# Kernel tuning notes

Measured on AMD Instinct MI355X. Metric: run time of the kernel, lower is better.

The kernel has to match this reference:

```python
import jax, jax.numpy as jnp
import numpy as np

NUM_EMBEDDINGS = 512
EMBEDDING_DIM = 64
COMMITMENT_COST = 0.25


def setup_inputs() -> dict:
    key = jax.random.key(0)
    k1, k2 = jax.random.split(key)
    inputs = jax.random.normal(k1, (64, 32, 32, EMBEDDING_DIM), dtype=jnp.float32)
    # nn.Embedding weight init: uniform(-1/K, 1/K)
    codebook = jax.random.uniform(
        k2, (NUM_EMBEDDINGS, EMBEDDING_DIM), dtype=jnp.float32,
        minval=-1.0 / NUM_EMBEDDINGS, maxval=1.0 / NUM_EMBEDDINGS)
    return {"inputs": inputs, "codebook": codebook}


def reference(inputs, codebook):
    D = codebook.shape[1]
    K = codebook.shape[0]
    flat = inputs.reshape(-1, D)  # [N, D]
    # Squared euclidean distances (argmin-equivalent to torch.cdist output)
    d2 = (jnp.sum(flat * flat, axis=1, keepdims=True)
          - 2.0 * (flat @ codebook.T)
          + jnp.sum(codebook * codebook, axis=1))  # [N, K]
    idx = jnp.argmin(d2, axis=1)  # [N]
    # Gather codebook rows (== one-hot @ codebook in the original)
    quantized = codebook[idx].reshape(inputs.shape)
    e_latent_loss = jnp.mean((jax.lax.stop_gradient(quantized) - inputs) ** 2)
    q_latent_loss = jnp.mean((quantized - jax.lax.stop_gradient(inputs)) ** 2)
    loss = q_latent_loss + COMMITMENT_COST * e_latent_loss
    # Straight-through estimator
    quantized_st = inputs + jax.lax.stop_gradient(quantized - inputs)
    # Perplexity from code usage histogram (== mean of one-hot encodings)
    n = flat.shape[0]
    avg_probs = jnp.zeros((K,), dtype=jnp.float32).at[idx].add(1.0) / n
    perplexity = jnp.exp(-jnp.sum(avg_probs * jnp.log(avg_probs + 1e-10)))
    encoding_indices = idx[:, None]  # [N, 1] to match torch unsqueeze(1)
    return (loss, quantized_st, perplexity, encoding_indices)
```

## Files before the change

kernel.cpp:

```cpp
#include <hip/hip_runtime.h>
#include <math.h>

#define K_EMB 512
#define DIM 64
#define NVEC 65536
#define OUT_LOSS 0
#define OUT_Q 1
#define OUT_PERP (1 + NVEC * DIM)
#define OUT_IDX (1 + NVEC * DIM + 1)
#define EPS2 1e-4f
#define FIX_CAP 16

typedef __attribute__((ext_vector_type(8))) short short8;
typedef __attribute__((ext_vector_type(4))) float float4v;


__device__ __forceinline__ unsigned short bf16_rn(float f) {
    unsigned u = __float_as_uint(f);
    return (unsigned short)((u + 0x7FFFu + ((u >> 16) & 1u)) >> 16);
}

__device__ __forceinline__ float np_pairwise8_sq(const float* v) {
    float r[8];
#pragma unroll
    for (int j = 0; j < 8; ++j) r[j] = __fmul_rn(v[j], v[j]);
#pragma unroll
    for (int i = 8; i < 64; i += 8) {
#pragma unroll
        for (int j = 0; j < 8; ++j) r[j] = __fadd_rn(r[j], __fmul_rn(v[i + j], v[i + j]));
    }
    return __fadd_rn(__fadd_rn(__fadd_rn(r[0], r[1]), __fadd_rn(r[2], r[3])),
                     __fadd_rn(__fadd_rn(r[4], r[5]), __fadd_rn(r[6], r[7])));
}

__global__ void vq_frag(const float* __restrict__ codebook, float* __restrict__ csq,
                        unsigned short* __restrict__ ahi, unsigned short* __restrict__ alo,
                        float4* __restrict__ csqf, unsigned* __restrict__ hist,
                        double* __restrict__ sse64) {
    const int id = blockIdx.x * 256 + threadIdx.x;
    const int t = id >> 7, step = (id >> 6) & 1, lane = id & 63;
    const int m = t * 16 + (lane & 15);
    const int kb = step * 32 + (lane >> 4) * 8;
    const float* src = codebook + (m << 6) + kb;
    short8 h, l;
#pragma unroll
    for (int j = 0; j < 8; ++j) {
        float f = src[j];
        unsigned short hv = bf16_rn(f);
        float lof = f - __uint_as_float(((unsigned)hv) << 16);
        h[j] = (short)hv;
        l[j] = (short)bf16_rn(lof);
    }
    const int fo = ((t * 2 + step) * 64 + lane) * 8;
    *(short8*)(ahi + fo) = h;
    *(short8*)(alo + fo) = l;
    if (step == 0) {
        const int k0 = t * 16 + (lane >> 4) * 4;
        csqf[t * 64 + lane] = make_float4(np_pairwise8_sq(codebook + (size_t)(k0 + 0) * 64),
                                          np_pairwise8_sq(codebook + (size_t)(k0 + 1) * 64),
                                          np_pairwise8_sq(codebook + (size_t)(k0 + 2) * 64),
                                          np_pairwise8_sq(codebook + (size_t)(k0 + 3) * 64));
    }
    if (id < 512) {
        csq[id] = np_pairwise8_sq(codebook + ((size_t)id << 6));
        hist[id] = 0u;
    }
    if (id >= 512 && id < 576) sse64[id - 512] = 0.0;
}

__launch_bounds__(256, 4)
__global__ void vq_main(const float* __restrict__ inputs, const float* __restrict__ codebook,
                        const float* __restrict__ csq, const unsigned short* __restrict__ ahi,
                        const unsigned short* __restrict__ alo, const float4* __restrict__ csqf,
                        unsigned* __restrict__ hist, double* __restrict__ sse64,
                        float* __restrict__ out) {
    __shared__ __align__(16) float s_x[64 * 68];
    __shared__ float s_A[64];
    __shared__ unsigned long long s_t1[4][64];
    __shared__ unsigned long long s_t2[4][64];
    __shared__ unsigned long long s_e[64];
    __shared__ int s_fix[FIX_CAP];
    __shared__ int s_nfix;
    __shared__ float s_w[4];

    const int tid = threadIdx.x;
    const int wave = tid >> 6, lane = tid & 63;
    const int vbase = blockIdx.x * 64;

    if (tid == 0) s_nfix = 0;

    {
        const float4* src = (const float4*)(inputs + ((size_t)vbase << 6));
#pragma unroll
        for (int i = 0; i < 4; ++i) {
            const int f = i * 256 + tid;
            float4 v = src[f];
            *(float4*)&s_x[(f >> 4) * 68 + (f & 15) * 4] = v;
        }
    }
    __syncthreads();

    if (tid < 64) s_A[tid] = np_pairwise8_sq(&s_x[tid * 68]);
    __syncthreads();

    short8 bhi[4][2], blo[4][2];
#pragma unroll
    for (int vt = 0; vt < 4; ++vt) {
        const int vrow = vt * 16 + (lane & 15);
#pragma unroll
        for (int step = 0; step < 2; ++step) {
            const int kb = step * 32 + (lane >> 4) * 8;
            float4 f0 = *(const float4*)&s_x[vrow * 68 + kb];
            float4 f1 = *(const float4*)&s_x[vrow * 68 + kb + 4];
            const float fs[8] = {f0.x, f0.y, f0.z, f0.w, f1.x, f1.y, f1.z, f1.w};
            short8 h, l;
#pragma unroll
            for (int j = 0; j < 8; ++j) {
                unsigned short hv = bf16_rn(fs[j]);
                float lof = fs[j] - __uint_as_float(((unsigned)hv) << 16);
                h[j] = (short)hv;
                l[j] = (short)bf16_rn(lof);
            }
            bhi[vt][step] = h;
            blo[vt][step] = l;
        }
    }

    unsigned long long e1[4] = {~0ULL, ~0ULL, ~0ULL, ~0ULL};
    unsigned long long e2[4] = {~0ULL, ~0ULL, ~0ULL, ~0ULL};

#pragma unroll 2
    for (int tt = 0; tt < 8; ++tt) {
        const int t = wave * 8 + tt;
        const int fo0 = ((t * 2 + 0) * 64 + lane) * 8;
        const int fo1 = ((t * 2 + 1) * 64 + lane) * 8;
        short8 ah0 = *(const short8*)(ahi + fo0);
        short8 ah1 = *(const short8*)(ahi + fo1);
        short8 al0 = *(const short8*)(alo + fo0);
        short8 al1 = *(const short8*)(alo + fo1);
        float4 cs = csqf[t * 64 + lane];
        const float csr[4] = {cs.x, cs.y, cs.z, cs.w};
#pragma unroll
        for (int vt = 0; vt < 4; ++vt) {
            float4v acc = {0.f, 0.f, 0.f, 0.f};
            acc = __builtin_amdgcn_mfma_f32_16x16x32_bf16(ah0, bhi[vt][0], acc, 0, 0, 0);
            acc = __builtin_amdgcn_mfma_f32_16x16x32_bf16(ah1, bhi[vt][1], acc, 0, 0, 0);
            acc = __builtin_amdgcn_mfma_f32_16x16x32_bf16(ah0, blo[vt][0], acc, 0, 0, 0);
            acc = __builtin_amdgcn_mfma_f32_16x16x32_bf16(ah1, blo[vt][1], acc, 0, 0, 0);
            acc = __builtin_amdgcn_mfma_f32_16x16x32_bf16(al0, bhi[vt][0], acc, 0, 0, 0);
            acc = __builtin_amdgcn_mfma_f32_16x16x32_bf16(al1, bhi[vt][1], acc, 0, 0, 0);
            const float Avt = s_A[vt * 16 + (lane & 15)];
#pragma unroll
            for (int r = 0; r < 4; ++r) {
                float d2 = __fadd_rn(__fsub_rn(Avt, __fmul_rn(2.0f, acc[r])), csr[r]);
                const unsigned k = (unsigned)(t * 16 + (lane >> 4) * 4 + r);
                unsigned long long e = ((unsigned long long)__float_as_uint(d2) << 32) | k;
                if (e < e1[vt]) { e2[vt] = e1[vt]; e1[vt] = e; }
                else if (e < e2[vt]) e2[vt] = e;
            }
        }
    }

#pragma unroll
    for (int vt = 0; vt < 4; ++vt) {
#pragma unroll
        for (int off = 16; off <= 32; off <<= 1) {
            unsigned long long o1 = __shfl_xor(e1[vt], off);
            unsigned long long o2 = __shfl_xor(e2[vt], off);
            if (o1 < e1[vt]) { e2[vt] = (e1[vt] < o2) ? e1[vt] : o2; e1[vt] = o1; }
            else if (o1 < e2[vt]) e2[vt] = o1;
        }
        if (lane < 16) {
            s_t1[wave][vt * 16 + lane] = e1[vt];
            s_t2[wave][vt * 16 + lane] = e2[vt];
        }
    }
    __syncthreads();

    if (tid < 64) {
        unsigned long long E1 = ~0ULL, E2 = ~0ULL;
#pragma unroll
        for (int w = 0; w < 4; ++w) {
            unsigned long long a = s_t1[w][tid], b = s_t2[w][tid];
            if (a < E1) { E2 = (E1 < b) ? E1 : b; E1 = a; }
            else if (a < E2) E2 = a;
        }
        s_e[tid] = E1;
        float b1 = __uint_as_float((unsigned)(E1 >> 32));
        float b2 = __uint_as_float((unsigned)(E2 >> 32));
        if (__fsub_rn(b2, b1) <= EPS2) {
            int pos = atomicAdd(&s_nfix, 1);
            if (pos < FIX_CAP) s_fix[pos] = tid;
        }
    }
    __syncthreads();

    {
        int nf = s_nfix; if (nf > FIX_CAP) nf = FIX_CAP;
        for (int f = wave; f < nf; f += 4) {
            const int vloc = s_fix[f];
            const float* xr = &s_x[vloc * 68];
            const float A = s_A[vloc];
            unsigned long long best = ~0ULL;
#pragma unroll 1
            for (int r8 = 0; r8 < 8; ++r8) {
                const int k = lane * 8 + r8;
                const float* c = codebook + (k << 6);
                float p[8] = {0.f, 0.f, 0.f, 0.f, 0.f, 0.f, 0.f, 0.f};
#pragma unroll
                for (int ii = 0; ii < 64; ii += 8)
#pragma unroll
                    for (int j = 0; j < 8; ++j)
                        p[j] = __builtin_fmaf(xr[ii + j], c[ii + j], p[j]);
                float dot = __fadd_rn(__fadd_rn(__fadd_rn(p[0], p[1]), __fadd_rn(p[2], p[3])),
                                      __fadd_rn(__fadd_rn(p[4], p[5]), __fadd_rn(p[6], p[7])));
                float d2 = __fadd_rn(__fsub_rn(A, __fmul_rn(2.0f, dot)), csq[k]);
                unsigned long long e = ((unsigned long long)__float_as_uint(d2) << 32) | (unsigned)k;
                if (e < best) best = e;
            }
#pragma unroll
            for (int off = 32; off > 0; off >>= 1) {
                unsigned long long o = __shfl_down(best, off);
                if (o < best) best = o;
            }
            if (lane == 0) s_e[vloc] = best;
        }
    }
    __syncthreads();

    if (tid < 64) {
        const unsigned kf = (unsigned)s_e[tid];
        out[OUT_IDX + vbase + tid] = (float)kf;
        atomicAdd(&hist[kf], 1u);
    }
    {
        float4* dst = (float4*)(out + OUT_Q + ((size_t)vbase << 6));
        float es = 0.f;
#pragma unroll
        for (int i = 0; i < 4; ++i) {
            const int f = i * 256 + tid;
            const int row = f >> 4, col = (f & 15) * 4;
            const unsigned k = (unsigned)s_e[row];
            float4 qv = *(const float4*)(codebook + ((size_t)k << 6) + col);
            dst[f] = qv;
            float4 xv = *(const float4*)&s_x[row * 68 + col];
            float d0 = qv.x - xv.x; es = __builtin_fmaf(d0, d0, es);
            float d1 = qv.y - xv.y; es = __builtin_fmaf(d1, d1, es);
            float d2 = qv.z - xv.z; es = __builtin_fmaf(d2, d2, es);
            float d3 = qv.w - xv.w; es = __builtin_fmaf(d3, d3, es);
        }
#pragma unroll
        for (int off = 32; off > 0; off >>= 1) es += __shfl_down(es, off);
        if (lane == 0) s_w[wave] = es;
    }
    __syncthreads();
    if (tid == 0)
        atomicAdd(&sse64[blockIdx.x & 63],
                  (double)(((s_w[0] + s_w[1]) + (s_w[2] + s_w[3]))));
}

__global__ void vq_final(const unsigned* __restrict__ hist, const double* __restrict__ sse64,
                         float* __restrict__ out) {
    __shared__ float s_wsm[8];
    const int k = threadIdx.x;
    float pr = (float)hist[k] / 65536.0f;
    float v = __fmul_rn(pr, logf(__fadd_rn(pr, 1e-10f)));
#pragma unroll
    for (int off = 32; off > 0; off >>= 1) v += __shfl_down(v, off);
    if ((k & 63) == 0) s_wsm[k >> 6] = v;
    __syncthreads();
    if (k == 0) {
        float S = 0.f;
#pragma unroll
        for (int i = 0; i < 8; ++i) S += s_wsm[i];
        out[OUT_PERP] = expf(-S);
        double sv = 0.0;
        for (int i = 0; i < 64; ++i) sv += sse64[i];
        float m = (float)(sv / 4194304.0);
        out[OUT_LOSS] = __fadd_rn(m, __fmul_rn(0.25f, m));
    }
}

extern "C" void kernel_launch(void* const* d_in, const int* in_sizes, int n_in,
                              void* d_out, int out_size, void* d_ws, size_t ws_size,
                              hipStream_t stream) {
    const float* inputs   = (const float*)d_in[0];
    const float* codebook = (const float*)d_in[1];
    float* out = (float*)d_out;
    float*          csq   = (float*)d_ws;
    double*         sse64 = (double*)((char*)d_ws + 2048);
    unsigned*       hist  = (unsigned*)((char*)d_ws + 2560);
    unsigned short* ahi   = (unsigned short*)((char*)d_ws + 4608);
    unsigned short* alo   = (unsigned short*)((char*)d_ws + 70144);
    float4*         csqf  = (float4*)((char*)d_ws + 135680);

    vq_frag<<<16, 256, 0, stream>>>(codebook, csq, ahi, alo, csqf, hist, sse64);
    vq_main<<<1024, 256, 0, stream>>>(inputs, codebook, csq, ahi, alo, csqf, hist, sse64, out);
    vq_final<<<1, 512, 0, stream>>>(hist, sse64, out);
}
```

Before: 155.1 us.

## Halve vectors per block in main kernel and split codebook prep into dedicated block

The main kernel now processes 32 vectors per block instead of 64 and launches twice as many blocks, so more blocks spread across the CUs. Each wave still streams all codebook fragments, so global/L2 traffic for codebook fragments doubles relative to the MFMA work. The prep kernel moves the codebook norm computation into a separate extra block that computes each norm once and builds the packed norm array from shared memory, instead of recomputing norms redundantly, and vectorises the fragment loads. The fixup path (not fully shown) presumably still works with the smaller tile.

```diff
diff --git a/kernel.cpp b/kernel.cpp
--- a/kernel.cpp
+++ b/kernel.cpp
@@ -37,35 +37,46 @@
                         unsigned short* __restrict__ ahi, unsigned short* __restrict__ alo,
                         float4* __restrict__ csqf, unsigned* __restrict__ hist,
                         double* __restrict__ sse64) {
-    const int id = blockIdx.x * 256 + threadIdx.x;
-    const int t = id >> 7, step = (id >> 6) & 1, lane = id & 63;
-    const int m = t * 16 + (lane & 15);
-    const int kb = step * 32 + (lane >> 4) * 8;
-    const float* src = codebook + (m << 6) + kb;
-    short8 h, l;
-#pragma unroll
-    for (int j = 0; j < 8; ++j) {
-        float f = src[j];
-        unsigned short hv = bf16_rn(f);
-        float lof = f - __uint_as_float(((unsigned)hv) << 16);
-        h[j] = (short)hv;
-        l[j] = (short)bf16_rn(lof);
-    }
-    const int fo = ((t * 2 + step) * 64 + lane) * 8;
-    *(short8*)(ahi + fo) = h;
-    *(short8*)(alo + fo) = l;
-    if (step == 0) {
-        const int k0 = t * 16 + (lane >> 4) * 4;
-        csqf[t * 64 + lane] = make_float4(np_pairwise8_sq(codebook + (size_t)(k0 + 0) * 64),
-                                          np_pairwise8_sq(codebook + (size_t)(k0 + 1) * 64),
-                                          np_pairwise8_sq(codebook + (size_t)(k0 + 2) * 64),
-                                          np_pairwise8_sq(codebook + (size_t)(k0 + 3) * 64));
-    }
-    if (id < 512) {
-        csq[id] = np_pairwise8_sq(codebook + ((size_t)id << 6));
-        hist[id] = 0u;
-    }
-    if (id >= 512 && id < 576) sse64[id - 512] = 0.0;
+    const int tid = threadIdx.x;
+    if (blockIdx.x < 16) {
+        const int id = blockIdx.x * 256 + tid;
+        const int t = id >> 7, step = (id >> 6) & 1, lane = id & 63;
+        const int m = t * 16 + (lane & 15);
+        const int kb = step * 32 + (lane >> 4) * 8;
+        const float4* src = (const float4*)(codebook + (m << 6) + kb);
+        float4 f0 = src[0], f1 = src[1];
+        const float fs[8] = {f0.x, f0.y, f0.z, f0.w, f1.x, f1.y, f1.z, f1.w};
+        short8 h, l;
+#pragma unroll
+        for (int j = 0; j < 8; ++j) {
+            unsigned short hv = bf16_rn(fs[j]);
+            float lof = fs[j] - __uint_as_float(((unsigned)hv) << 16);
+            h[j] = (short)hv;
+            l[j] = (short)bf16_rn(lof);
+        }
+        const int fo = ((t * 2 + step) * 64 + lane) * 8;
+        *(short8*)(ahi + fo) = h;
+        *(short8*)(alo + fo) = l;
+    } else {
+        __shared__ float s_csq[512];
+#pragma unroll
+        for (int r = 0; r < 2; ++r) {
+            const int k = tid + 256 * r;
+            float v = np_pairwise8_sq(codebook + ((size_t)k << 6));
+            s_csq[k] = v;
+            csq[k] = v;
+            hist[k] = 0u;
+        }
+        if (tid < 64) sse64[tid] = 0.0;
+        __syncthreads();
+#pragma unroll
+        for (int i = 0; i < 8; ++i) {
+            const int id = i * 256 + tid;
+            const int t = id >> 6, lane = id & 63;
+            const int k0 = t * 16 + (lane >> 4) * 4;
+            csqf[id] = make_float4(s_csq[k0], s_csq[k0 + 1], s_csq[k0 + 2], s_csq[k0 + 3]);
+        }
+    }
 }
 
 __launch_bounds__(256, 4)
@@ -74,25 +85,25 @@
                         const unsigned short* __restrict__ alo, const float4* __restrict__ csqf,
                         unsigned* __restrict__ hist, double* __restrict__ sse64,
                         float* __restrict__ out) {
-    __shared__ __align__(16) float s_x[64 * 68];
-    __shared__ float s_A[64];
-    __shared__ unsigned long long s_t1[4][64];
-    __shared__ unsigned long long s_t2[4][64];
-    __shared__ unsigned long long s_e[64];
+    __shared__ __align__(16) float s_x[32 * 68];
+    __shared__ float s_A[32];
+    __shared__ unsigned long long s_t1[4][32];
+    __shared__ unsigned long long s_t2[4][32];
+    __shared__ unsigned long long s_e[32];
     __shared__ int s_fix[FIX_CAP];
     __shared__ int s_nfix;
     __shared__ float s_w[4];
 
     const int tid = threadIdx.x;
     const int wave = tid >> 6, lane = tid & 63;
-    const int vbase = blockIdx.x * 64;
+    const int vbase = blockIdx.x * 32;
 
     if (tid == 0) s_nfix = 0;
 
     {
         const float4* src = (const float4*)(inputs + ((size_t)vbase << 6));
 #pragma unroll
-        for (int i = 0; i < 4; ++i) {
+        for (int i = 0; i < 2; ++i) {
             const int f = i * 256 + tid;
             float4 v = src[f];
             *(float4*)&s_x[(f >> 4) * 68 + (f & 15) * 4] = v;
@@ -100,12 +111,12 @@
     }
     __syncthreads();
 
-    if (tid < 64) s_A[tid] = np_pairwise8_sq(&s_x[tid * 68]);
-    __syncthreads();
-
-    short8 bhi[4][2], blo[4][2];
-#pragma unroll
-    for (int vt = 0; vt < 4; ++vt) {
+    if (tid < 32) s_A[tid] = np_pairwise8_sq(&s_x[tid * 68]);
+    __syncthreads();
+
+    short8 bhi[2][2], blo[2][2];
+#pragma unroll
+    for (int vt = 0; vt < 2; ++vt) {
         const int vrow = vt * 16 + (lane & 15);
 #pragma unroll
         for (int step = 0; step < 2; ++step) {
@@ -126,8 +137,7 @@
         }
     }
 
-    unsigned long long e1[4] = {~0ULL, ~0ULL, ~0ULL, ~0ULL};
-    unsigned long long e2[4] = {~0ULL, ~0ULL, ~0ULL, ~0ULL};
+    unsigned long long e1[2] = {~0ULL, ~0ULL}, e2[2] = {~0ULL, ~0ULL};
 
 #pragma unroll 2
     for (int tt = 0; tt < 8; ++tt) {
@@ -141,7 +151,7 @@
         float4 cs = csqf[t * 64 + lane];
         const float csr[4] = {cs.x, cs.y, cs.z, cs.w};
 #pragma unroll
-        for (int vt = 0; vt < 4; ++vt) {
+        for (int vt = 0; vt < 2; ++vt) {
             float4v acc = {0.f, 0.f, 0.f, 0.f};
             acc = __builtin_amdgcn_mfma_f32_16x16x32_bf16(ah0, bhi[vt][0], acc, 0, 0, 0);
             acc = __builtin_amdgcn_mfma_f32_16x16x32_bf16(ah1, bhi[vt][1], acc, 0, 0, 0);
@@ -162,7 +172,7 @@
     }
 
 #pragma unroll
-    for (int vt = 0; vt < 4; ++vt) {
+    for (int vt = 0; vt < 2; ++vt) {
 #pragma unroll
         for (int off = 16; off <= 32; off <<= 1) {
             unsigned long long o1 = __shfl_xor(e1[vt], off);
@@ -177,7 +187,7 @@
     }
     __syncthreads();
 
-    if (tid < 64) {
+    if (tid < 32) {
         unsigned long long E1 = ~0ULL, E2 = ~0ULL;
 #pragma unroll
         for (int w = 0; w < 4; ++w) {
@@ -228,7 +238,7 @@
     }
     __syncthreads();
 
-    if (tid < 64) {
+    if (tid < 32) {
         const unsigned kf = (unsigned)s_e[tid];
         out[OUT_IDX + vbase + tid] = (float)kf;
         atomicAdd(&hist[kf], 1u);
@@ -237,7 +247,7 @@
         float4* dst = (float4*)(out + OUT_Q + ((size_t)vbase << 6));
         float es = 0.f;
 #pragma unroll
-        for (int i = 0; i < 4; ++i) {
+        for (int i = 0; i < 2; ++i) {
             const int f = i * 256 + tid;
             const int row = f >> 4, col = (f & 15) * 4;
             const unsigned k = (unsigned)s_e[row];
@@ -294,7 +304,7 @@
     unsigned short* alo   = (unsigned short*)((char*)d_ws + 70144);
     float4*         csqf  = (float4*)((char*)d_ws + 135680);
 
-    vq_frag<<<16, 256, 0, stream>>>(codebook, csq, ahi, alo, csqf, hist, sse64);
-    vq_main<<<1024, 256, 0, stream>>>(inputs, codebook, csq, ahi, alo, csqf, hist, sse64, out);
+    vq_frag<<<17, 256, 0, stream>>>(codebook, csq, ahi, alo, csqf, hist, sse64);
+    vq_main<<<2048, 256, 0, stream>>>(inputs, codebook, csq, ahi, alo, csqf, hist, sse64, out);
     vq_final<<<1, 512, 0, stream>>>(hist, sse64, out);
 }
```

Result: faster. 137.2 us (-11.6%).
